# Optimization experiments

Hardware: AMD Instinct MI355X
Metric: run time of the kernel (lower is better)

The kernel has to match this reference:

```python
import jax, jax.numpy as jnp
import numpy as np

B, NUM_TATUMS, F, T = 8, 256, 128, 2048


def repeat_with_tatums(features, tatum_frames, total_frames):
    """Vectorized equivalent of per-sample repeat_interleave + pad_sequence.
    features: (B, num_tatums, F); tatum_frames: (B, num_tatums+1) monotone.
    Frame t of sample i takes tatum j with tatum_frames[i,j] <= t < tatum_frames[i,j+1];
    frames >= tatum_frames[i,-1] are zero padding.
    """
    num_tatums = features.shape[1]
    t = jnp.arange(total_frames)

    def per_sample(f, tf):
        idx = jnp.searchsorted(tf[1:], t, side='right')  # (T,)
        idx = jnp.clip(idx, 0, num_tatums - 1)
        valid = t < tf[-1]
        return jnp.where(valid[:, None], f[idx], jnp.zeros((), f.dtype))

    return jax.vmap(per_sample)(features, tatum_frames)  # (B, T, F)


def conv2d_same(x, w, b):
    y = jax.lax.conv_general_dilated(
        x, w, window_strides=(1, 1), padding='SAME',
        dimension_numbers=('NCHW', 'OIHW', 'NCHW'))
    return y + b[None, :, None, None]


def setup_inputs() -> dict:
    key = jax.random.key(0)
    ks = jax.random.split(key, 12)
    pitch_rendered = jax.random.normal(ks[0], (B, NUM_TATUMS, F), dtype=jnp.float32)
    onset = jax.random.uniform(ks[1], (B, NUM_TATUMS), dtype=jnp.float32)
    tf = jnp.sort(jax.random.randint(ks[2], (B, NUM_TATUMS + 1), 0, T), axis=1)
    tf = tf.at[:, 0].set(0).at[:, -1].set(T)  # boundaries: start 0, end T
    tatum_frames = tf.astype(jnp.int64)
    s = 0.1
    W1 = jax.random.normal(ks[3], (32, 2, 3, 3), dtype=jnp.float32) * s
    b1 = jnp.zeros((32,), jnp.float32)
    W2 = jax.random.normal(ks[4], (32, 32, 3, 3), dtype=jnp.float32) * s
    b2 = jnp.zeros((32,), jnp.float32)
    W3 = jax.random.normal(ks[5], (32, 32, 3, 3), dtype=jnp.float32) * s
    b3 = jnp.zeros((32,), jnp.float32)
    W4 = jax.random.normal(ks[6], (1, 32, 3, 3), dtype=jnp.float32) * s
    b4 = jnp.zeros((1,), jnp.float32)
    return dict(pitch_rendered=pitch_rendered, onset=onset, tatum_frames=tatum_frames,
                W1=W1, b1=b1, W2=W2, b2=b2, W3=W3, b3=b3, W4=W4, b4=b4)


def reference(pitch_rendered, onset, tatum_frames, W1, b1, W2, b2, W3, b3, W4, b4):
    num_features = pitch_rendered.shape[-1]
    pr = repeat_with_tatums(pitch_rendered, tatum_frames, T)            # (B, T, F)
    on = repeat_with_tatums(jnp.broadcast_to(onset[:, :, None], onset.shape + (num_features,)),
                            tatum_frames, T)                             # (B, T, F)
    x = jnp.stack([pr, on], axis=1)                                      # (B, 2, T, F)
    x = jax.nn.relu(conv2d_same(x, W1, b1))
    x = jax.nn.relu(conv2d_same(x, W2, b2))
    x = jax.nn.relu(conv2d_same(x, W3, b3))
    x = conv2d_same(x, W4, b4)                                           # (B, 1, T, F)
    return jnp.squeeze(x, axis=1)                                        # (B, T, F)
```

## Files before the change

### kernel.cpp

```cpp
#include <hip/hip_runtime.h>
#include <hip/hip_bf16.h>

#define TDIM 2048
#define FDIM 128
#define NWAVES 8

typedef __attribute__((ext_vector_type(8))) short short8;
typedef __attribute__((ext_vector_type(4))) float f32x4;
typedef __attribute__((ext_vector_type(4))) unsigned uint4v;

__device__ __forceinline__ unsigned short f2bf(float v) {
    __bf16 h = (__bf16)v;
    return __builtin_bit_cast(unsigned short, h);
}

__global__ void prep_weights_kernel(const float* __restrict__ W1, const float* __restrict__ W2,
                                    const float* __restrict__ W3, const float* __restrict__ W4,
                                    unsigned short* __restrict__ wt)
{
    for (int e = blockIdx.x * 256 + threadIdx.x; e < 24064; e += gridDim.x * 256) {
        float v = 0.0f;
        if (e < 1024) {
            int cot = e >> 9, kb = (e >> 7) & 3, co16 = (e >> 3) & 15, ee = e & 7;
            int k = kb * 8 + ee, uv = k >> 1, ch = k & 1, co = cot * 16 + co16;
            if (uv < 9) v = W1[co * 18 + ch * 9 + uv];
        } else if (e < 10240) {
            int q = e - 1024;
            int g = q / 2304, r = q % 2304;
            int uv = r >> 8, co = (r >> 3) & 31, ci = g * 8 + (r & 7);
            v = W2[co * 288 + ci * 9 + uv];
        } else if (e < 19456) {
            int q = e - 10240;
            int g = q / 2304, r = q % 2304;
            int uv = r >> 8, co = (r >> 3) & 31, ci = g * 8 + (r & 7);
            v = W3[co * 288 + ci * 9 + uv];
        } else {
            int q = e - 19456;
            int g = q / 1152, r = q % 1152;
            int uv = r >> 7, co = (r >> 3) & 15, ci = g * 8 + (r & 7);
            if (co == 0) v = W4[ci * 9 + uv];
        }
        wt[e] = f2bf(v);
    }
}

__device__ __forceinline__ uint2 pack4(f32x4 c, bool valid) {
    unsigned short h[4];
#pragma unroll
    for (int k = 0; k < 4; ++k) {
        float v = fmaxf(c[k], 0.0f);
        h[k] = valid ? f2bf(v) : (unsigned short)0;
    }
    uint2 r;
    r.x = (unsigned)h[0] | ((unsigned)h[1] << 16);
    r.y = (unsigned)h[2] | ((unsigned)h[3] << 16);
    return r;
}

template<int WI, int WO, int PSI, int PSO, bool EDGE>
__device__ __forceinline__ void conv_mid(const char* __restrict__ inb, char* __restrict__ outb,
                                         const char* __restrict__ wlds, const float* __restrict__ bias,
                                         int wave, int lane, int t_base, int f_base)
{
    const int lm = lane & 15, g = lane >> 4;
    const char* wp = wlds + g * 4608;
    short8 wa0[9], wa1[9];
#pragma unroll
    for (int uv = 0; uv < 9; ++uv) {
        wa0[uv] = *(const short8*)(wp + (uv * 32 + lm) * 16);
        wa1[uv] = *(const short8*)(wp + (uv * 32 + 16 + lm) * 16);
    }
    f32x4 bias0 = *(const f32x4*)(bias + g * 4);
    f32x4 bias1 = *(const f32x4*)(bias + 16 + g * 4);
    const f32x4 zero = {0.0f, 0.0f, 0.0f, 0.0f};

    const char* inp = inb + g * PSI;
    constexpr int NPX = WO * WO;
    constexpr int NG = (NPX + 15) / 16;
    for (int grp = wave; grp < NG; grp += NWAVES) {
        int m = grp * 16 + lm;
        bool mv = m < NPX;
        int mc = mv ? m : NPX - 1;
        int i = mc / WO, j = mc - i * WO;
        const char* base = inp + (i * WI + j) * 16;
        f32x4 c0a = bias0, c0b = zero, c1a = bias1, c1b = zero;
#pragma unroll
        for (int uv = 0; uv < 9; ++uv) {
            int u = uv / 3, v = uv - u * 3;
            short8 bf = *(const short8*)(base + (u * WI + v) * 16);
            if (uv < 5) {
                c0a = __builtin_amdgcn_mfma_f32_16x16x32_bf16(wa0[uv], bf, c0a, 0, 0, 0);
                c1a = __builtin_amdgcn_mfma_f32_16x16x32_bf16(wa1[uv], bf, c1a, 0, 0, 0);
            } else {
                c0b = __builtin_amdgcn_mfma_f32_16x16x32_bf16(wa0[uv], bf, c0b, 0, 0, 0);
                c1b = __builtin_amdgcn_mfma_f32_16x16x32_bf16(wa1[uv], bf, c1b, 0, 0, 0);
            }
        }
        if (mv) {
            bool valid = true;
            if (EDGE) {
                int t = t_base + i, f = f_base + j;
                valid = (t >= 0) && (t < TDIM) && (f >= 0) && (f < FDIM);
            }
            char* wb = outb + (g >> 1) * PSO + m * 16 + (g & 1) * 8;
            *(uint2*)wb             = pack4(c0a + c0b, valid);
            *(uint2*)(wb + 2 * PSO) = pack4(c1a + c1b, valid);
        }
    }
}

template<bool EDGE>
__global__ __launch_bounds__(512, 4)
void fused_mfma_kernel(const float* __restrict__ pr, const float* __restrict__ onset,
                       const int* __restrict__ tf,
                       const float* __restrict__ b1, const float* __restrict__ b2,
                       const float* __restrict__ b3, const float* __restrict__ b4,
                       const unsigned short* __restrict__ wt, float* __restrict__ out)
{
    __shared__ __attribute__((aligned(16))) char lds[77312];

    const int tid = threadIdx.x;
    const int lane = tid & 63, wave = tid >> 6;
    int f0, t0;
    if (EDGE) {
        int id = blockIdx.x;
        int bx, by;
        if (id < 128)      { bx = 0; by = id; }
        else if (id < 256) { bx = 7; by = id - 128; }
        else {
            int q = id - 256;
            if (q < 6) { bx = 1 + q; by = 0; }
            else       { bx = 1 + (q - 6); by = 127; }
        }
        f0 = bx * 16; t0 = by * 16;
    } else {
        f0 = (blockIdx.x + 1) * 16;
        t0 = (blockIdx.y + 1) * 16;
    }
    const int b = blockIdx.z;

    unsigned* X4 = (unsigned*)lds;
    char* Y2 = lds + 2304;
    char* Y1 = lds + 27904;
    char* Y3 = lds + 27904;
    char* WB = lds + 58880;
    const char* wtb = (const char*)wt;

    for (int ch = tid; ch < 1152; ch += 512)
        *(short8*)(WB + ch * 16) = *(const short8*)(wtb + 2048 + ch * 16);

    for (int p = tid; p < 576; p += 512) {
        int i = p / 24, j = p - (p / 24) * 24;
        int t = t0 - 4 + i, f = f0 - 4 + j;
        unsigned xv = 0u;
        bool valid = true;
        if (EDGE) valid = (t >= 0) && (t < TDIM) && (f >= 0) && (f < FDIM);
        if (valid) {
            const int* a = tf + b * 257 + 1;
            int pos = 0;
#pragma unroll
            for (int step = 128; step >= 1; step >>= 1) {
                pos += (a[pos + step - 1] <= t) ? step : 0;
            }
            int idx = pos < 255 ? pos : 255;
            float v0 = pr[(b * 256 + idx) * 128 + f];
            float v1 = onset[b * 256 + idx];
            xv = (unsigned)f2bf(v0) | ((unsigned)f2bf(v1) << 16);
        }
        X4[p] = xv;
    }
    __syncthreads();

    const int lm = lane & 15, g = lane >> 4;

    {
        const short8 waA = *(const short8*)(wtb + (g * 16 + lm) * 16);
        const short8 waB = *(const short8*)(wtb + (64 + g * 16 + lm) * 16);
        int off4[4];
#pragma unroll
        for (int q = 0; q < 4; ++q) {
            int uv = g * 4 + q;
            int uvc = uv <= 8 ? uv : 8;
            int u = uvc / 3, v = uvc - u * 3;
            off4[q] = u * 24 + v;
        }
        f32x4 bias0 = *(const f32x4*)(b1 + g * 4);
        f32x4 bias1 = *(const f32x4*)(b1 + 16 + g * 4);

        constexpr int NPX = 22 * 22;
        constexpr int NG = (NPX + 15) / 16;
        for (int grp = wave; grp < NG; grp += NWAVES) {
            int m = grp * 16 + lm;
            bool mv = m < NPX;
            int mc = mv ? m : NPX - 1;
            int i = mc / 22, j = mc - i * 22;
            int base4 = i * 24 + j;
            uint4v bu;
#pragma unroll
            for (int q = 0; q < 4; ++q) bu[q] = X4[base4 + off4[q]];
            short8 bf = __builtin_bit_cast(short8, bu);
            f32x4 c0 = __builtin_amdgcn_mfma_f32_16x16x32_bf16(waA, bf, bias0, 0, 0, 0);
            f32x4 c1 = __builtin_amdgcn_mfma_f32_16x16x32_bf16(waB, bf, bias1, 0, 0, 0);
            if (mv) {
                bool valid = true;
                if (EDGE) {
                    int t = t0 - 3 + i, f = f0 - 3 + j;
                    valid = (t >= 0) && (t < TDIM) && (f >= 0) && (f < FDIM);
                }
                char* wb = Y1 + (g >> 1) * 7744 + m * 16 + (g & 1) * 8;
                *(uint2*)wb           = pack4(c0, valid);
                *(uint2*)(wb + 15488) = pack4(c1, valid);
            }
        }
    }

    short8 w3p0 = *(const short8*)(wtb + 20480 + tid * 16);
    short8 w3p1 = *(const short8*)(wtb + 20480 + (tid + 512) * 16);
    short8 w3p2;
    if (tid < 128) w3p2 = *(const short8*)(wtb + 20480 + (tid + 1024) * 16);
    __syncthreads();

    conv_mid<22, 20, 7744, 6400, EDGE>(Y1, Y2, WB, b2, wave, lane, t0 - 2, f0 - 2);
    __syncthreads();

    *(short8*)(WB + tid * 16) = w3p0;
    *(short8*)(WB + (tid + 512) * 16) = w3p1;
    if (tid < 128) *(short8*)(WB + (tid + 1024) * 16) = w3p2;
    __syncthreads();

    short8 w4p0 = *(const short8*)(wtb + 38912 + tid * 16);
    short8 w4p1;
    if (tid < 64) w4p1 = *(const short8*)(wtb + 38912 + (tid + 512) * 16);

    conv_mid<20, 18, 6400, 5184, EDGE>(Y2, Y3, WB, b3, wave, lane, t0 - 1, f0 - 1);
    __syncthreads();

    *(short8*)(WB + tid * 16) = w4p0;
    if (tid < 64) *(short8*)(WB + (tid + 512) * 16) = w4p1;
    __syncthreads();

    {
        const char* wp = WB + g * 2304;
        short8 wa[9];
#pragma unroll
        for (int uv = 0; uv < 9; ++uv)
            wa[uv] = *(const short8*)(wp + (uv * 16 + lm) * 16);
        float bv = b4[0];
        const char* yp = Y3 + g * 5184;
        const f32x4 zero = {0.0f, 0.0f, 0.0f, 0.0f};
        for (int grp = wave; grp < 16; grp += NWAVES) {
            const char* base = yp + (grp * 18 + lm) * 16;
            f32x4 ca = zero, cb = zero;
#pragma unroll
            for (int uv = 0; uv < 9; ++uv) {
                int u = uv / 3, v = uv - u * 3;
                short8 bf = *(const short8*)(base + (u * 18 + v) * 16);
                if (uv < 5) ca = __builtin_amdgcn_mfma_f32_16x16x32_bf16(wa[uv], bf, ca, 0, 0, 0);
                else        cb = __builtin_amdgcn_mfma_f32_16x16x32_bf16(wa[uv], bf, cb, 0, 0, 0);
            }
            if (g == 0)
                out[((long)b * TDIM + (t0 + grp)) * FDIM + f0 + lm] = ca[0] + cb[0] + bv;
        }
    }
}

extern "C" void kernel_launch(void* const* d_in, const int* in_sizes, int n_in,
                              void* d_out, int out_size, void* d_ws, size_t ws_size,
                              hipStream_t stream) {
    const float* pr    = (const float*)d_in[0];
    const float* onset = (const float*)d_in[1];
    const int*   tf    = (const int*)d_in[2];
    const float* W1 = (const float*)d_in[3];
    const float* B1 = (const float*)d_in[4];
    const float* W2 = (const float*)d_in[5];
    const float* B2 = (const float*)d_in[6];
    const float* W3 = (const float*)d_in[7];
    const float* B3 = (const float*)d_in[8];
    const float* W4 = (const float*)d_in[9];
    const float* B4 = (const float*)d_in[10];
    float* out = (float*)d_out;
    unsigned short* wt = (unsigned short*)d_ws;

    prep_weights_kernel<<<32, 256, 0, stream>>>(W1, W2, W3, W4, wt);

    dim3 gridI(6, 126, 8);
    fused_mfma_kernel<false><<<gridI, 512, 0, stream>>>(pr, onset, tf, B1, B2, B3, B4, wt, out);

    dim3 gridE(268, 1, 8);
    fused_mfma_kernel<true><<<gridE, 512, 0, stream>>>(pr, onset, tf, B1, B2, B3, B4, wt, out);
}
```

Measured before the change: 251.6 us.

## Load conv weights from global directly and merge edge/interior launches into one

Conv weights for layers 2-4 are now read from global memory (through cache) straight into registers instead of being staged in LDS. This removes the staging stores and the extra barriers between layers. Dropping the weight buffer shrinks LDS per block, which may let more blocks fit per CU. The separate interior and edge kernels are merged into one launch with a runtime edge flag, removing a launch but adding per-pixel edge branching to every block.

Result: slower. 261.2 us (+3.8%).

```diff
diff --git a/kernel.cpp b/kernel.cpp
--- a/kernel.cpp
+++ b/kernel.cpp
@@ -57,18 +57,19 @@
     return r;
 }
 
-template<int WI, int WO, int PSI, int PSO, bool EDGE>
+template<int WI, int WO, int PSI, int PSO>
 __device__ __forceinline__ void conv_mid(const char* __restrict__ inb, char* __restrict__ outb,
-                                         const char* __restrict__ wlds, const float* __restrict__ bias,
-                                         int wave, int lane, int t_base, int f_base)
+                                         const unsigned short* __restrict__ wg,
+                                         const float* __restrict__ bias,
+                                         int wave, int lane, int t_base, int f_base, bool edge)
 {
     const int lm = lane & 15, g = lane >> 4;
-    const char* wp = wlds + g * 4608;
+    const unsigned short* wp = wg + g * 2304 + lm * 8;
     short8 wa0[9], wa1[9];
 #pragma unroll
     for (int uv = 0; uv < 9; ++uv) {
-        wa0[uv] = *(const short8*)(wp + (uv * 32 + lm) * 16);
-        wa1[uv] = *(const short8*)(wp + (uv * 32 + 16 + lm) * 16);
+        wa0[uv] = *(const short8*)(wp + uv * 256);
+        wa1[uv] = *(const short8*)(wp + uv * 256 + 128);
     }
     f32x4 bias0 = *(const f32x4*)(bias + g * 4);
     f32x4 bias1 = *(const f32x4*)(bias + 16 + g * 4);
@@ -98,7 +99,7 @@
         }
         if (mv) {
             bool valid = true;
-            if (EDGE) {
+            if (edge) {
                 int t = t_base + i, f = f_base + j;
                 valid = (t >= 0) && (t < TDIM) && (f >= 0) && (f < FDIM);
             }
@@ -109,7 +110,6 @@
     }
 }
 
-template<bool EDGE>
 __global__ __launch_bounds__(512, 4)
 void fused_mfma_kernel(const float* __restrict__ pr, const float* __restrict__ onset,
                        const int* __restrict__ tf,
@@ -117,44 +117,28 @@
                        const float* __restrict__ b3, const float* __restrict__ b4,
                        const unsigned short* __restrict__ wt, float* __restrict__ out)
 {
-    __shared__ __attribute__((aligned(16))) char lds[77312];
+    __shared__ __attribute__((aligned(16))) char lds[56576];
 
     const int tid = threadIdx.x;
     const int lane = tid & 63, wave = tid >> 6;
-    int f0, t0;
-    if (EDGE) {
-        int id = blockIdx.x;
-        int bx, by;
-        if (id < 128)      { bx = 0; by = id; }
-        else if (id < 256) { bx = 7; by = id - 128; }
-        else {
-            int q = id - 256;
-            if (q < 6) { bx = 1 + q; by = 0; }
-            else       { bx = 1 + (q - 6); by = 127; }
-        }
-        f0 = bx * 16; t0 = by * 16;
-    } else {
-        f0 = (blockIdx.x + 1) * 16;
-        t0 = (blockIdx.y + 1) * 16;
-    }
-    const int b = blockIdx.z;
+    const int f0 = blockIdx.x * 16;
+    const int t0 = blockIdx.y * 16;
+    const int b  = blockIdx.z;
+    const bool edge = (blockIdx.x == 0) || (blockIdx.x == 7) ||
+                      (blockIdx.y == 0) || (blockIdx.y == 127);
 
     unsigned* X4 = (unsigned*)lds;
-    char* Y2 = lds + 2304;
-    char* Y1 = lds + 27904;
-    char* Y3 = lds + 27904;
-    char* WB = lds + 58880;
+    char* Y2 = lds;
+    char* Y1 = lds + 25600;
+    char* Y3 = lds + 25600;
     const char* wtb = (const char*)wt;
-
-    for (int ch = tid; ch < 1152; ch += 512)
-        *(short8*)(WB + ch * 16) = *(const short8*)(wtb + 2048 + ch * 16);
 
     for (int p = tid; p < 576; p += 512) {
         int i = p / 24, j = p - (p / 24) * 24;
         int t = t0 - 4 + i, f = f0 - 4 + j;
         unsigned xv = 0u;
         bool valid = true;
-        if (EDGE) valid = (t >= 0) && (t < TDIM) && (f >= 0) && (f < FDIM);
+        if (edge) valid = (t >= 0) && (t < TDIM) && (f >= 0) && (f < FDIM);
         if (valid) {
             const int* a = tf + b * 257 + 1;
             int pos = 0;
@@ -203,7 +187,7 @@
             f32x4 c1 = __builtin_amdgcn_mfma_f32_16x16x32_bf16(waB, bf, bias1, 0, 0, 0);
             if (mv) {
                 bool valid = true;
-                if (EDGE) {
+                if (edge) {
                     int t = t0 - 3 + i, f = f0 - 3 + j;
                     valid = (t >= 0) && (t < TDIM) && (f >= 0) && (f < FDIM);
                 }
@@ -213,38 +197,20 @@
             }
         }
     }
-
-    short8 w3p0 = *(const short8*)(wtb + 20480 + tid * 16);
-    short8 w3p1 = *(const short8*)(wtb + 20480 + (tid + 512) * 16);
-    short8 w3p2;
-    if (tid < 128) w3p2 = *(const short8*)(wtb + 20480 + (tid + 1024) * 16);
-    __syncthreads();
-
-    conv_mid<22, 20, 7744, 6400, EDGE>(Y1, Y2, WB, b2, wave, lane, t0 - 2, f0 - 2);
-    __syncthreads();
-
-    *(short8*)(WB + tid * 16) = w3p0;
-    *(short8*)(WB + (tid + 512) * 16) = w3p1;
-    if (tid < 128) *(short8*)(WB + (tid + 1024) * 16) = w3p2;
-    __syncthreads();
-
-    short8 w4p0 = *(const short8*)(wtb + 38912 + tid * 16);
-    short8 w4p1;
-    if (tid < 64) w4p1 = *(const short8*)(wtb + 38912 + (tid + 512) * 16);
-
-    conv_mid<20, 18, 6400, 5184, EDGE>(Y2, Y3, WB, b3, wave, lane, t0 - 1, f0 - 1);
-    __syncthreads();
-
-    *(short8*)(WB + tid * 16) = w4p0;
-    if (tid < 64) *(short8*)(WB + (tid + 512) * 16) = w4p1;
+    __syncthreads();
+
+    conv_mid<22, 20, 7744, 6400>(Y1, Y2, wt + 1024,  b2, wave, lane, t0 - 2, f0 - 2, edge);
+    __syncthreads();
+
+    conv_mid<20, 18, 6400, 5184>(Y2, Y3, wt + 10240, b3, wave, lane, t0 - 1, f0 - 1, edge);
     __syncthreads();
 
     {
-        const char* wp = WB + g * 2304;
+        const unsigned short* wp = wt + 19456 + g * 1152 + lm * 8;
         short8 wa[9];
 #pragma unroll
         for (int uv = 0; uv < 9; ++uv)
-            wa[uv] = *(const short8*)(wp + (uv * 16 + lm) * 16);
+            wa[uv] = *(const short8*)(wp + uv * 128);
         float bv = b4[0];
         const char* yp = Y3 + g * 5184;
         const f32x4 zero = {0.0f, 0.0f, 0.0f, 0.0f};
@@ -283,9 +249,6 @@
 
     prep_weights_kernel<<<32, 256, 0, stream>>>(W1, W2, W3, W4, wt);
 
-    dim3 gridI(6, 126, 8);
-    fused_mfma_kernel<false><<<gridI, 512, 0, stream>>>(pr, onset, tf, B1, B2, B3, B4, wt, out);
-
-    dim3 gridE(268, 1, 8);
-    fused_mfma_kernel<true><<<gridE, 512, 0, stream>>>(pr, onset, tf, B1, B2, B3, B4, wt, out);
-}
+    dim3 grid(8, 128, 8);
+    fused_mfma_kernel<<<grid, 512, 0, stream>>>(pr, onset, tf, B1, B2, B3, B4, wt, out);
+}
```
